# Kernel optimization log

Measured on AMD Instinct MI355X. Metric: run time of the kernel, lower is better.

## Reference

```python
import jax, jax.numpy as jnp
import numpy as np

NUM_CLASSES = 2
TOP_K = 200
CONF_THRESH = 0.01
NMS_THRESH = 0.45
VAR0, VAR1 = 0.1, 0.2
NUM_PRIORS = 72192
BATCH = 64


def setup_inputs() -> dict:
    key = jax.random.key(0)
    k1, k2, k3 = jax.random.split(key, 3)
    loc_data = jax.random.normal(k1, (BATCH, NUM_PRIORS, 4), dtype=jnp.float32)
    conf_data = jax.random.uniform(k2, (BATCH * NUM_PRIORS, NUM_CLASSES), dtype=jnp.float32)
    prior_data = jax.random.uniform(k3, (NUM_PRIORS, 4), dtype=jnp.float32) * 0.5 + 0.01
    return {"loc_data": loc_data, "conf_data": conf_data, "prior_data": prior_data}


def decode(loc, priors):
    # loc, priors: [P, 4] (cx, cy, w, h) -> corners (x1, y1, x2, y2)
    cxcy = priors[:, :2] + loc[:, :2] * VAR0 * priors[:, 2:]
    wh = priors[:, 2:] * jnp.exp(loc[:, 2:] * VAR1)
    return jnp.concatenate([cxcy - wh / 2, cxcy + wh / 2], axis=-1)


def pairwise_iou(boxes):
    # boxes: [K, 4] corners
    area = (boxes[:, 2] - boxes[:, 0]) * (boxes[:, 3] - boxes[:, 1])
    lt = jnp.maximum(boxes[:, None, :2], boxes[None, :, :2])
    rb = jnp.minimum(boxes[:, None, 2:], boxes[None, :, 2:])
    wh = jnp.clip(rb - lt, 0.0)
    inter = wh[..., 0] * wh[..., 1]
    union = area[:, None] + area[None, :] - inter
    return inter / jnp.maximum(union, 1e-12)


def nms_single(boxes, scores):
    # boxes: [P,4], scores: [P] -> [TOP_K, 5] rows (score, x1, y1, x2, y2)
    masked = jnp.where(scores > CONF_THRESH, scores, -jnp.inf)
    top_scores, idx = jax.lax.top_k(masked, TOP_K)      # descending, like torch nms
    cand_boxes = boxes[idx]                              # [K,4]
    valid = top_scores > CONF_THRESH
    iou = pairwise_iou(cand_boxes)                       # [K,K]
    ar = jnp.arange(TOP_K)

    def body(i, keep):
        sup = (iou[i] > NMS_THRESH) & (ar > i)
        return jnp.where(keep[i], keep & ~sup, keep)

    keep = jax.lax.fori_loop(0, TOP_K, body, valid)
    # compact kept detections to the front (matches output[i, cl, :count] = ...)
    pos = jnp.cumsum(keep) - 1
    pos = jnp.where(keep, pos, TOP_K)                    # dropped rows scatter out of range
    rows = jnp.concatenate([top_scores[:, None], cand_boxes], axis=1)
    return jnp.zeros((TOP_K, 5), dtype=boxes.dtype).at[pos].set(rows, mode="drop")


def reference(loc_data, conf_data, prior_data):
    num = loc_data.shape[0]
    num_priors = prior_data.shape[0]
    conf_preds = conf_data.reshape(num, num_priors, NUM_CLASSES)  # [B, P, C]
    decoded = jax.vmap(decode, in_axes=(0, None))(loc_data, prior_data)  # [B, P, 4]
    per_class = []
    # class 0 is background -> zeros (matches torch output init)
    per_class.append(jnp.zeros((num, TOP_K, 5), dtype=loc_data.dtype))
    for cl in range(1, NUM_CLASSES):
        per_class.append(jax.vmap(nms_single)(decoded, conf_preds[:, :, cl]))
    # final rank-based zeroing in torch source is a no-op (fill_ on an advanced-index copy)
    return jnp.stack(per_class, axis=1)  # [B, C, TOP_K, 5]
```

## Files before the change

kernel.cpp:

```cpp
#include <hip/hip_runtime.h>
#include <math.h>

#pragma clang fp contract(off)

#define NUM_PRIORS 72192
#define BATCH      64
#define TOPK       200
#define CONF_TH    0.01f
#define NMS_TH     0.45f
#define NBINS      256
#define SLICES     32
#define ROWS       (NUM_PRIORS / SLICES)
#define Q4         (ROWS / 2)
#define QB         (NUM_PRIORS / 2)
#define CAPS       64
#define CAP        1024
#define KW         7
#define NMS_NTH    1024
#define B255       0.99609375f

typedef unsigned long long u64;

__device__ __forceinline__ int bin_of(float s) {
    int b = (int)(s * 256.0f);
    return b > 255 ? 255 : b;
}

__global__ __launch_bounds__(256) void collect255_kernel(const float* __restrict__ conf,
                                                         unsigned* __restrict__ scnt,
                                                         u64* __restrict__ cand) {
    __shared__ unsigned lcnt;
    const int b = blockIdx.y, slice = blockIdx.x, tid = threadIdx.x;
    if (tid == 0) lcnt = 0;
    __syncthreads();
    const float4* c4 = (const float4*)conf;
    const long base4 = (long)b * QB + (long)slice * Q4;
    const int prow0 = slice * ROWS;
    u64* seg = cand + ((long)b * SLICES + slice) * CAPS;

    float4 v0 = c4[base4 + tid];
    float4 v1 = c4[base4 + tid + 256];
    float4 v2 = c4[base4 + tid + 512];
    float4 v3 = c4[base4 + tid + 768];

#define P255(sv, pidx)                                                          \
    do {                                                                        \
        float s_ = (sv);                                                        \
        if (s_ >= B255) {                                                       \
            unsigned pos = atomicAdd(&lcnt, 1u);                                \
            if (pos < CAPS)                                                     \
                seg[pos] = ((u64)__float_as_uint(s_) << 32) |                   \
                           (u64)(0xFFFFFFFFu - (unsigned)(pidx));               \
        }                                                                       \
    } while (0)

    P255(v0.y, prow0 + 2 * tid);
    P255(v0.w, prow0 + 2 * tid + 1);
    P255(v1.y, prow0 + 2 * (tid + 256));
    P255(v1.w, prow0 + 2 * (tid + 256) + 1);
    P255(v2.y, prow0 + 2 * (tid + 512));
    P255(v2.w, prow0 + 2 * (tid + 512) + 1);
    P255(v3.y, prow0 + 2 * (tid + 768));
    P255(v3.w, prow0 + 2 * (tid + 768) + 1);
    if (tid < Q4 - 1024) {
        float4 vt = c4[base4 + tid + 1024];
        P255(vt.y, prow0 + 2 * (tid + 1024));
        P255(vt.w, prow0 + 2 * (tid + 1024) + 1);
    }
#undef P255
    __syncthreads();
    if (tid == 0) scnt[b * SLICES + slice] = lcnt;
}

__global__ __launch_bounds__(NMS_NTH, 4) void nms_kernel(const float* __restrict__ loc,
                           const float* __restrict__ prior,
                           const float* __restrict__ conf,
                           const unsigned* __restrict__ scnt,
                           u64* __restrict__ cand,
                           float* __restrict__ out) {
    __shared__ alignas(16) u64 keys[CAP];
    __shared__ float4 bbox[224];
    __shared__ float bsc_s[TOPK];
    __shared__ alignas(16) unsigned invR[TOPK][8];
    __shared__ unsigned kw0[8];
    __shared__ unsigned kwF[KW];
    __shared__ int soff[SLICES + 1];
    __shared__ int scl[SLICES];
    __shared__ unsigned histc[NBINS];
    __shared__ unsigned lcnt32[SLICES];
    __shared__ int TshC, needfix;
    const int b = blockIdx.x, tid = threadIdx.x;

    if (tid < 64) {
        int s = tid;
        unsigned cs = (s < SLICES) ? scnt[b * SLICES + s] : 0u;
        int c = (cs < CAPS) ? (int)cs : CAPS;
        int v = c;
#pragma unroll
        for (int d = 1; d < 32; d <<= 1) {
            int o = __shfl_up(v, d);
            if ((int)tid >= d) v += o;
        }
        unsigned tot = cs;
#pragma unroll
        for (int d = 32; d >= 1; d >>= 1) tot += __shfl_xor(tot, d);
        u64 ovb = __ballot(cs > CAPS);
        if (s < SLICES) {
            int P = v - c;
            int off = P > CAP ? CAP : P;
            int rem = CAP - off;
            int cl = c < rem ? c : rem;
            soff[s] = off;
            scl[s] = cl;
            if (s == SLICES - 1) soff[SLICES] = (P + c > CAP) ? CAP : (P + c);
        }
        if (tid == 0) {
            needfix = (tot < TOPK) || (ovb != 0ull);
            TshC = 0;
        }
    }
    {
        float* ob = out + (long)b * 2 * TOPK * 5;
        for (int i = tid; i < 2 * TOPK * 5; i += NMS_NTH) ob[i] = 0.f;
    }
    if (tid < 8) kw0[tid] = 0u;
    __syncthreads();

    if (needfix) {
        const float4* c4 = (const float4*)conf;
        for (int i = tid; i < NBINS; i += NMS_NTH) histc[i] = 0u;
        __syncthreads();
        for (int q = tid; q < QB; q += NMS_NTH) {
            float4 v = c4[(long)b * QB + q];
            if (v.y > CONF_TH) atomicAdd(&histc[bin_of(v.y)], 1u);
            if (v.w > CONF_TH) atomicAdd(&histc[bin_of(v.w)], 1u);
        }
        __syncthreads();
        for (int off = 1; off < NBINS; off <<= 1) {
            unsigned vv = 0u;
            if (tid < NBINS && tid + off < NBINS) vv = histc[tid + off];
            __syncthreads();
            if (tid < NBINS) histc[tid] += vv;
            __syncthreads();
        }
        if (tid < NBINS) {
            unsigned s0 = histc[tid];
            unsigned sn = (tid + 1 < NBINS) ? histc[tid + 1] : 0u;
            if (s0 >= TOPK && (tid == NBINS - 1 || sn < TOPK)) TshC = tid;
        }
        if (tid < SLICES) lcnt32[tid] = 0u;
        __syncthreads();
        const int T = TshC;
        for (int q = tid; q < QB; q += NMS_NTH) {
            float4 v = c4[(long)b * QB + q];
            int sl = q / Q4;
            u64* seg = cand + ((long)b * SLICES + sl) * CAPS;
            if (v.y > CONF_TH && bin_of(v.y) >= T) {
                unsigned pos = atomicAdd(&lcnt32[sl], 1u);
                if (pos < CAPS)
                    seg[pos] = ((u64)__float_as_uint(v.y) << 32) |
                               (u64)(0xFFFFFFFFu - (unsigned)(2 * q));
            }
            if (v.w > CONF_TH && bin_of(v.w) >= T) {
                unsigned pos = atomicAdd(&lcnt32[sl], 1u);
                if (pos < CAPS)
                    seg[pos] = ((u64)__float_as_uint(v.w) << 32) |
                               (u64)(0xFFFFFFFFu - (unsigned)(2 * q + 1));
            }
        }
        __syncthreads();
        if (tid < 64) {
            int s = tid;
            unsigned cs = (s < SLICES) ? lcnt32[s] : 0u;
            int c = (cs < CAPS) ? (int)cs : CAPS;
            int v = c;
#pragma unroll
            for (int d = 1; d < 32; d <<= 1) {
                int o = __shfl_up(v, d);
                if ((int)tid >= d) v += o;
            }
            if (s < SLICES) {
                int P = v - c;
                int off = P > CAP ? CAP : P;
                int rem = CAP - off;
                int cl = c < rem ? c : rem;
                soff[s] = off;
                scl[s] = cl;
                if (s == SLICES - 1) soff[SLICES] = (P + c > CAP) ? CAP : (P + c);
            }
        }
        __syncthreads();
    }

    const int n = soff[SLICES];
    const int nn = (n + 15) & ~15;
    for (int pos = tid; pos < SLICES * CAPS; pos += NMS_NTH) {
        int s = pos >> 6, idx = pos & 63;
        if (idx < scl[s])
            keys[soff[s] + idx] = cand[((long)b * SLICES + s) * CAPS + idx];
    }
    for (int i = n + tid; i < nn; i += NMS_NTH) keys[i] = 0ull;
    __syncthreads();

    u64 kc = (tid < n) ? keys[tid] : 0ull;
    int rk = 0;
    if ((int)(tid & ~63u) < n) {
        const uint4* k4 = (const uint4*)keys;
        for (int k = 0; k < nn; k += 16) {
            uint4 q[8];
#pragma unroll
            for (int j = 0; j < 8; j++) q[j] = k4[(k >> 1) + j];
#pragma unroll
            for (int j = 0; j < 8; j++) {
                u64 a = ((u64)q[j].y << 32) | (u64)q[j].x;
                u64 c = ((u64)q[j].w << 32) | (u64)q[j].z;
                rk += (a > kc) ? 1 : 0;
                rk += (c > kc) ? 1 : 0;
            }
        }
    }
    if (tid < n && rk < TOPK) {
        u64 key = kc;
        float sc = __uint_as_float((unsigned)(key >> 32));
        unsigned p = 0xFFFFFFFFu - (unsigned)(key & 0xFFFFFFFFull);
        float4 l4 = ((const float4*)loc)[(long)b * NUM_PRIORS + p];
        float4 p4 = ((const float4*)prior)[p];
        float cx = p4.x + (l4.x * 0.1f) * p4.z;
        float cy = p4.y + (l4.y * 0.1f) * p4.w;
        float w_ = p4.z * (float)exp((double)(l4.z * 0.2f));
        float h_ = p4.w * (float)exp((double)(l4.w * 0.2f));
        float x1 = cx - w_ * 0.5f, y1 = cy - h_ * 0.5f;
        float x2 = cx + w_ * 0.5f, y2 = cy + h_ * 0.5f;
        bsc_s[rk] = sc;
        bbox[rk] = make_float4(x1, y1, x2, y2);
        atomicOr(&kw0[rk >> 5], 1u << (rk & 31));
    }
    __syncthreads();

    {
        const int q = tid >> 8, i = tid & 255;
        if (i < TOPK) {
            const float4 ib = bbox[i];
            const float iar = (ib.z - ib.x) * (ib.w - ib.y);
#pragma unroll
            for (int wi = 0; wi < 2; wi++) {
                if (wi == 1 && q == 3) break;
                const int w = (wi == 0) ? q : q + 4;
                const int jbase = w * 32;
                unsigned inv = 0xFFFFFFFFu;
#pragma unroll
                for (int g = 0; g < 32; g += 8) {
                    float4 J[8];
#pragma unroll
                    for (int r = 0; r < 8; r++) J[r] = bbox[jbase + g + r];
#pragma unroll
                    for (int r = 0; r < 8; r++) {
                        const int j = jbase + g + r;
                        if (j > i && j < TOPK) {
                            float4 jb = J[r];
                            float jar = (jb.z - jb.x) * (jb.w - jb.y);
                            float ltx = fmaxf(ib.x, jb.x);
                            float lty = fmaxf(ib.y, jb.y);
                            float rbx = fminf(ib.z, jb.z);
                            float rby = fminf(ib.w, jb.w);
                            float wx = fmaxf(rbx - ltx, 0.0f);
                            float wy = fmaxf(rby - lty, 0.0f);
                            float inter = wx * wy;
                            float uni = fmaxf((iar + jar) - inter, 1e-12f);
                            float t045 = uni * NMS_TH;
                            bool sup = inter > t045 * 1.000001f;
                            bool amb = (inter >= t045 * 0.999999f) && !sup;
                            if (__builtin_expect(amb, 0)) {
                                sup = (inter / uni) > NMS_TH;
                            }
                            if (sup) inv &= ~(1u << (g + r));
                        }
                    }
                }
                invR[i][w] = inv;
            }
        }
    }
    __syncthreads();

    if (tid < 64) {
        unsigned kk0 = kw0[0], kk1 = kw0[1], kk2 = kw0[2], kk3 = kw0[3];
        unsigned kk4 = kw0[4], kk5 = kw0[5], kk6 = kw0[6];
        const uint4* iv4 = (const uint4*)invR;
#define GSTEP(W, KKW)                                                           \
        {                                                                       \
            unsigned live = (KKW);                                              \
            while (live) {                                                      \
                int t = __ffs(live) - 1;                                        \
                int i = (W) * 32 + t;                                           \
                uint4 A = iv4[2 * i];                                           \
                uint4 C = iv4[2 * i + 1];                                       \
                kk0 &= A.x; kk1 &= A.y; kk2 &= A.z; kk3 &= A.w;                 \
                kk4 &= C.x; kk5 &= C.y; kk6 &= C.z;                             \
                unsigned above = ~((2u << t) - 1u);             \
                live = (KKW) & above;                                           \
            }                                                                   \
        }
        GSTEP(0, kk0); GSTEP(1, kk1); GSTEP(2, kk2); GSTEP(3, kk3);
        GSTEP(4, kk4); GSTEP(5, kk5); GSTEP(6, kk6);
#undef GSTEP
        if (tid == 0) {
            kwF[0] = kk0; kwF[1] = kk1; kwF[2] = kk2; kwF[3] = kk3;
            kwF[4] = kk4; kwF[5] = kk5; kwF[6] = kk6;
        }
    }
    __syncthreads();

    if (tid < TOPK) {
        const int wsel = tid >> 5, bsel = tid & 31;
        if ((kwF[wsel] >> bsel) & 1u) {
            int pos = 0;
#pragma unroll
            for (int w = 0; w < KW; w++) {
                unsigned kw_ = kwF[w];
                if (w < wsel) pos += __popc(kw_);
                else if (w == wsel) pos += __popc(kw_ & ((bsel == 0) ? 0u : (0xFFFFFFFFu >> (32 - bsel))));
            }
            float4 jb = bbox[tid];
            float* o = out + (((long)b * 2 + 1) * TOPK + pos) * 5;
            o[0] = bsc_s[tid];
            o[1] = jb.x;
            o[2] = jb.y;
            o[3] = jb.z;
            o[4] = jb.w;
        }
    }
}

extern "C" void kernel_launch(void* const* d_in, const int* in_sizes, int n_in,
                              void* d_out, int out_size, void* d_ws, size_t ws_size,
                              hipStream_t stream) {
    const float* loc   = (const float*)d_in[0];
    const float* conf  = (const float*)d_in[1];
    const float* prior = (const float*)d_in[2];
    float* out = (float*)d_out;

    char* w = (char*)d_ws;
    unsigned* scnt = (unsigned*)w;
    u64* cand      = (u64*)(w + 8192);

    collect255_kernel<<<dim3(SLICES, BATCH), 256, 0, stream>>>(conf, scnt, cand);
    nms_kernel<<<BATCH, NMS_NTH, 0, stream>>>(loc, prior, conf, scnt, cand, out);
}
```

Baseline: 35.26 us.

## Fuse candidate collection into NMS kernel with direct shared-memory append

Removes the separate collect kernel and its global candidate workspace. Each 1024-thread block now scans its whole batch row of confidences itself and appends scores at or above the top bin straight into the shared key array with one shared atomic counter. This drops a kernel launch and the global round trip, but only 64 blocks now read the full confidence tensor, so parallelism for the streaming pass falls from 2048 blocks to 64.

```diff
diff --git a/kernel.cpp b/kernel.cpp
--- a/kernel.cpp
+++ b/kernel.cpp
@@ -9,14 +9,9 @@
 #define CONF_TH    0.01f
 #define NMS_TH     0.45f
 #define NBINS      256
-#define SLICES     32
-#define ROWS       (NUM_PRIORS / SLICES)
-#define Q4         (ROWS / 2)
 #define QB         (NUM_PRIORS / 2)
-#define CAPS       64
 #define CAP        1024
 #define KW         7
-#define NMS_NTH    1024
 #define B255       0.99609375f
 
 typedef unsigned long long u64;
@@ -26,57 +21,9 @@
     return b > 255 ? 255 : b;
 }
 
-__global__ __launch_bounds__(256) void collect255_kernel(const float* __restrict__ conf,
-                                                         unsigned* __restrict__ scnt,
-                                                         u64* __restrict__ cand) {
-    __shared__ unsigned lcnt;
-    const int b = blockIdx.y, slice = blockIdx.x, tid = threadIdx.x;
-    if (tid == 0) lcnt = 0;
-    __syncthreads();
-    const float4* c4 = (const float4*)conf;
-    const long base4 = (long)b * QB + (long)slice * Q4;
-    const int prow0 = slice * ROWS;
-    u64* seg = cand + ((long)b * SLICES + slice) * CAPS;
-
-    float4 v0 = c4[base4 + tid];
-    float4 v1 = c4[base4 + tid + 256];
-    float4 v2 = c4[base4 + tid + 512];
-    float4 v3 = c4[base4 + tid + 768];
-
-#define P255(sv, pidx)                                                          \
-    do {                                                                        \
-        float s_ = (sv);                                                        \
-        if (s_ >= B255) {                                                       \
-            unsigned pos = atomicAdd(&lcnt, 1u);                                \
-            if (pos < CAPS)                                                     \
-                seg[pos] = ((u64)__float_as_uint(s_) << 32) |                   \
-                           (u64)(0xFFFFFFFFu - (unsigned)(pidx));               \
-        }                                                                       \
-    } while (0)
-
-    P255(v0.y, prow0 + 2 * tid);
-    P255(v0.w, prow0 + 2 * tid + 1);
-    P255(v1.y, prow0 + 2 * (tid + 256));
-    P255(v1.w, prow0 + 2 * (tid + 256) + 1);
-    P255(v2.y, prow0 + 2 * (tid + 512));
-    P255(v2.w, prow0 + 2 * (tid + 512) + 1);
-    P255(v3.y, prow0 + 2 * (tid + 768));
-    P255(v3.w, prow0 + 2 * (tid + 768) + 1);
-    if (tid < Q4 - 1024) {
-        float4 vt = c4[base4 + tid + 1024];
-        P255(vt.y, prow0 + 2 * (tid + 1024));
-        P255(vt.w, prow0 + 2 * (tid + 1024) + 1);
-    }
-#undef P255
-    __syncthreads();
-    if (tid == 0) scnt[b * SLICES + slice] = lcnt;
-}
-
-__global__ __launch_bounds__(NMS_NTH, 4) void nms_kernel(const float* __restrict__ loc,
+__global__ __launch_bounds__(1024, 4) void fused_kernel(const float* __restrict__ loc,
                            const float* __restrict__ prior,
                            const float* __restrict__ conf,
-                           const unsigned* __restrict__ scnt,
-                           u64* __restrict__ cand,
                            float* __restrict__ out) {
     __shared__ alignas(16) u64 keys[CAP];
     __shared__ float4 bbox[224];
@@ -84,61 +31,75 @@
     __shared__ alignas(16) unsigned invR[TOPK][8];
     __shared__ unsigned kw0[8];
     __shared__ unsigned kwF[KW];
-    __shared__ int soff[SLICES + 1];
-    __shared__ int scl[SLICES];
+    __shared__ unsigned lcnt, lcnt2;
     __shared__ unsigned histc[NBINS];
-    __shared__ unsigned lcnt32[SLICES];
-    __shared__ int TshC, needfix;
+    __shared__ int TshC;
+
     const int b = blockIdx.x, tid = threadIdx.x;
 
-    if (tid < 64) {
-        int s = tid;
-        unsigned cs = (s < SLICES) ? scnt[b * SLICES + s] : 0u;
-        int c = (cs < CAPS) ? (int)cs : CAPS;
-        int v = c;
-#pragma unroll
-        for (int d = 1; d < 32; d <<= 1) {
-            int o = __shfl_up(v, d);
-            if ((int)tid >= d) v += o;
-        }
-        unsigned tot = cs;
-#pragma unroll
-        for (int d = 32; d >= 1; d >>= 1) tot += __shfl_xor(tot, d);
-        u64 ovb = __ballot(cs > CAPS);
-        if (s < SLICES) {
-            int P = v - c;
-            int off = P > CAP ? CAP : P;
-            int rem = CAP - off;
-            int cl = c < rem ? c : rem;
-            soff[s] = off;
-            scl[s] = cl;
-            if (s == SLICES - 1) soff[SLICES] = (P + c > CAP) ? CAP : (P + c);
-        }
-        if (tid == 0) {
-            needfix = (tot < TOPK) || (ovb != 0ull);
-            TshC = 0;
-        }
-    }
+    if (tid == 0) { lcnt = 0u; lcnt2 = 0u; TshC = 0; }
+    if (tid >= 8 && tid < 16) kw0[tid - 8] = 0u;
+    if (tid >= 32 && tid < 56) bbox[200 + (tid - 32)] = make_float4(0.f, 0.f, 0.f, 0.f);
     {
-        float* ob = out + (long)b * 2 * TOPK * 5;
-        for (int i = tid; i < 2 * TOPK * 5; i += NMS_NTH) ob[i] = 0.f;
-    }
-    if (tid < 8) kw0[tid] = 0u;
-    __syncthreads();
-
-    if (needfix) {
-        const float4* c4 = (const float4*)conf;
-        for (int i = tid; i < NBINS; i += NMS_NTH) histc[i] = 0u;
-        __syncthreads();
-        for (int q = tid; q < QB; q += NMS_NTH) {
-            float4 v = c4[(long)b * QB + q];
+        float* ob = out + (long)b * (2 * TOPK * 5);
+        ob[tid] = 0.f;
+        if (tid < 2 * TOPK * 5 - 1024) ob[tid + 1024] = 0.f;
+    }
+    __syncthreads();
+
+    const float4* c4 = (const float4*)conf + (long)b * QB;
+#define APPEND(sv, pidx)                                                        \
+    do {                                                                        \
+        float s_ = (sv);                                                        \
+        if (s_ >= B255) {                                                       \
+            unsigned pos = atomicAdd(&lcnt, 1u);                                \
+            if (pos < CAP)                                                      \
+                keys[pos] = ((u64)__float_as_uint(s_) << 32) |                  \
+                            (u64)(0xFFFFFFFFu - (unsigned)(pidx));              \
+        }                                                                       \
+    } while (0)
+    int base = 0;
+    for (int it = 0; it < 8; ++it, base += 4096) {
+        float4 v0 = c4[base + tid];
+        float4 v1 = c4[base + 1024 + tid];
+        float4 v2 = c4[base + 2048 + tid];
+        float4 v3 = c4[base + 3072 + tid];
+        APPEND(v0.y, 2 * (base + tid));        APPEND(v0.w, 2 * (base + tid) + 1);
+        APPEND(v1.y, 2 * (base + 1024 + tid)); APPEND(v1.w, 2 * (base + 1024 + tid) + 1);
+        APPEND(v2.y, 2 * (base + 2048 + tid)); APPEND(v2.w, 2 * (base + 2048 + tid) + 1);
+        APPEND(v3.y, 2 * (base + 3072 + tid)); APPEND(v3.w, 2 * (base + 3072 + tid) + 1);
+    }
+    {
+        float4 v0 = c4[base + tid];
+        float4 v1 = c4[base + 1024 + tid];
+        float4 v2 = c4[base + 2048 + tid];
+        APPEND(v0.y, 2 * (base + tid));        APPEND(v0.w, 2 * (base + tid) + 1);
+        APPEND(v1.y, 2 * (base + 1024 + tid)); APPEND(v1.w, 2 * (base + 1024 + tid) + 1);
+        APPEND(v2.y, 2 * (base + 2048 + tid)); APPEND(v2.w, 2 * (base + 2048 + tid) + 1);
+    }
+    if (tid < QB - 35840) {
+        float4 vt = c4[35840 + tid];
+        APPEND(vt.y, 2 * (35840 + tid));
+        APPEND(vt.w, 2 * (35840 + tid) + 1);
+    }
+#undef APPEND
+    __syncthreads();
+
+    const unsigned total = lcnt;
+    int n;
+    if (total >= TOPK && total <= CAP) {
+        n = (int)total;
+    } else {
+        if (tid < NBINS) histc[tid] = 0u;
+        __syncthreads();
+        for (int q = tid; q < QB; q += 1024) {
+            float4 v = c4[q];
             if (v.y > CONF_TH) atomicAdd(&histc[bin_of(v.y)], 1u);
             if (v.w > CONF_TH) atomicAdd(&histc[bin_of(v.w)], 1u);
         }
         __syncthreads();
         for (int off = 1; off < NBINS; off <<= 1) {
-            unsigned vv = 0u;
-            if (tid < NBINS && tid + off < NBINS) vv = histc[tid + off];
+            unsigned vv = (tid < NBINS && tid + off < NBINS) ? histc[tid + off] : 0u;
             __syncthreads();
             if (tid < NBINS) histc[tid] += vv;
             __syncthreads();
@@ -148,58 +109,30 @@
             unsigned sn = (tid + 1 < NBINS) ? histc[tid + 1] : 0u;
             if (s0 >= TOPK && (tid == NBINS - 1 || sn < TOPK)) TshC = tid;
         }
-        if (tid < SLICES) lcnt32[tid] = 0u;
         __syncthreads();
         const int T = TshC;
-        for (int q = tid; q < QB; q += NMS_NTH) {
-            float4 v = c4[(long)b * QB + q];
-            int sl = q / Q4;
-            u64* seg = cand + ((long)b * SLICES + sl) * CAPS;
+        for (int q = tid; q < QB; q += 1024) {
+            float4 v = c4[q];
             if (v.y > CONF_TH && bin_of(v.y) >= T) {
-                unsigned pos = atomicAdd(&lcnt32[sl], 1u);
-                if (pos < CAPS)
-                    seg[pos] = ((u64)__float_as_uint(v.y) << 32) |
-                               (u64)(0xFFFFFFFFu - (unsigned)(2 * q));
+                unsigned pos = atomicAdd(&lcnt2, 1u);
+                if (pos < CAP)
+                    keys[pos] = ((u64)__float_as_uint(v.y) << 32) |
+                                (u64)(0xFFFFFFFFu - (unsigned)(2 * q));
             }
             if (v.w > CONF_TH && bin_of(v.w) >= T) {
-                unsigned pos = atomicAdd(&lcnt32[sl], 1u);
-                if (pos < CAPS)
-                    seg[pos] = ((u64)__float_as_uint(v.w) << 32) |
-                               (u64)(0xFFFFFFFFu - (unsigned)(2 * q + 1));
-            }
-        }
-        __syncthreads();
-        if (tid < 64) {
-            int s = tid;
-            unsigned cs = (s < SLICES) ? lcnt32[s] : 0u;
-            int c = (cs < CAPS) ? (int)cs : CAPS;
-            int v = c;
-#pragma unroll
-            for (int d = 1; d < 32; d <<= 1) {
-                int o = __shfl_up(v, d);
-                if ((int)tid >= d) v += o;
-            }
-            if (s < SLICES) {
-                int P = v - c;
-                int off = P > CAP ? CAP : P;
-                int rem = CAP - off;
-                int cl = c < rem ? c : rem;
-                soff[s] = off;
-                scl[s] = cl;
-                if (s == SLICES - 1) soff[SLICES] = (P + c > CAP) ? CAP : (P + c);
-            }
-        }
-        __syncthreads();
-    }
-
-    const int n = soff[SLICES];
+                unsigned pos = atomicAdd(&lcnt2, 1u);
+                if (pos < CAP)
+                    keys[pos] = ((u64)__float_as_uint(v.w) << 32) |
+                                (u64)(0xFFFFFFFFu - (unsigned)(2 * q + 1));
+            }
+        }
+        __syncthreads();
+        unsigned t2 = lcnt2;
+        n = (t2 < CAP) ? (int)t2 : CAP;
+    }
+
     const int nn = (n + 15) & ~15;
-    for (int pos = tid; pos < SLICES * CAPS; pos += NMS_NTH) {
-        int s = pos >> 6, idx = pos & 63;
-        if (idx < scl[s])
-            keys[soff[s] + idx] = cand[((long)b * SLICES + s) * CAPS + idx];
-    }
-    for (int i = n + tid; i < nn; i += NMS_NTH) keys[i] = 0ull;
+    for (int i = n + tid; i < nn; i += 1024) keys[i] = 0ull;
     __syncthreads();
 
     u64 kc = (tid < n) ? keys[tid] : 0ull;
@@ -340,10 +273,5 @@
     const float* prior = (const float*)d_in[2];
     float* out = (float*)d_out;
 
-    char* w = (char*)d_ws;
-    unsigned* scnt = (unsigned*)w;
-    u64* cand      = (u64*)(w + 8192);
-
-    collect255_kernel<<<dim3(SLICES, BATCH), 256, 0, stream>>>(conf, scnt, cand);
-    nms_kernel<<<BATCH, NMS_NTH, 0, stream>>>(loc, prior, conf, scnt, cand, out);
+    fused_kernel<<<BATCH, 1024, 0, stream>>>(loc, prior, conf, out);
 }
```

Measured after the change: 43.82 us. 24.3% more time.
